# Kernel tuning notes

Measured on AMD Instinct MI355X. Metric: run time of the kernel, lower is better.

## Reference

```python
import jax, jax.numpy as jnp
import numpy as np

B, S, D, NQ, NC, MC, K = 64, 200, 128, 50000, 1000, 4, 10
N = NQ + NC  # total graph nodes (concepts first, then questions, matching torch concat order)


def setup_inputs() -> dict:
    key = jax.random.key(0)
    ks = jax.random.split(key, 32)
    f = lambda i, shape: jax.random.normal(ks[i], shape, dtype=jnp.float32) * 0.02
    return {
        "emb_q": f(0, (NQ, D)), "emb_c": f(1, (NC, D)), "emb_r": f(2, (2, D)),
        "Wih1": f(3, (3 * D, 2 * D)), "Whh1": f(4, (3 * D, D)), "bih1": f(5, (3 * D,)), "bhh1": f(6, (3 * D,)),
        "Wih2": f(7, (3 * D, D)), "Whh2": f(8, (3 * D, D)), "bih2": f(9, (3 * D,)), "bhh2": f(10, (3 * D,)),
        "Wg1": f(11, (D, D)), "Wg2": f(12, (D, D)), "Wg3": f(13, (D, D)),
        "Wagg": f(14, (D, D)), "bagg": f(15, (D,)),
        "Wq": f(16, (D, D)), "bq": f(17, (D,)),
        "Wk": f(18, (D, D)), "bk": f(19, (D,)),
        "Ww": f(20, (1, 2 * D)), "bw": f(21, (1,)),
        "question_seq": jax.random.randint(ks[22], (B, S), 0, NQ),
        "correct_seq": jax.random.randint(ks[23], (B, S), 0, 2),
        "mask_seq": jnp.ones((B, S), dtype=jnp.int32),
        "q_table": jax.random.randint(ks[24], (NQ, MC), 0, NC),
    }


def _gru(x, h, Wih, Whh, bih, bhh):
    gi = x @ Wih.T + bih
    gh = h @ Whh.T + bhh
    i_r, i_z, i_n = jnp.split(gi, 3, axis=-1)
    h_r, h_z, h_n = jnp.split(gh, 3, axis=-1)
    r = jax.nn.sigmoid(i_r + h_r)
    z = jax.nn.sigmoid(i_z + h_z)
    n = jnp.tanh(i_n + r * h_n)
    return (1.0 - z) * n + z * h


def _sage_mean(x, src, dst, W):
    # SAGEConv4GIKT (eval): out = lin_r(mean_agg_over_neighbors + x), lin_r has no bias.
    agg = jax.ops.segment_sum(x[dst], src, num_segments=N)
    cnt = jax.ops.segment_sum(jnp.ones((src.shape[0], 1), x.dtype), src, num_segments=N)
    agg = agg / jnp.maximum(cnt, 1.0)
    return (agg + x) @ W.T


def reference(emb_q, emb_c, emb_r, Wih1, Whh1, bih1, bhh1, Wih2, Whh2, bih2, bhh2,
              Wg1, Wg2, Wg3, Wagg, bagg, Wq, bq, Wk, bk, Ww, bw,
              question_seq, correct_seq, mask_seq, q_table):
    # ---- GNN propagation over the full question-concept bipartite graph ----
    x = jnp.concatenate([emb_c, emb_q], axis=0)  # [N, D], concepts first
    q_glob = jnp.repeat(jnp.arange(NQ, dtype=q_table.dtype) + NC, MC)  # question global ids
    c_glob = q_table.reshape(-1)                                       # concept global ids
    x = _sage_mean(x, q_glob, c_glob, Wg1)  # q2c: aggregate at questions from concepts
    x = _sage_mean(x, c_glob, q_glob, Wg2)  # c2q: aggregate at concepts from questions
    x = _sage_mean(x, q_glob, c_glob, Wg3)  # q2c again
    x = jnp.tanh(x @ Wagg.T + bagg)

    tgrid = jnp.arange(S)

    def step(carry, inp):
        h1, h2, keyhist, statehist = carry
        t, q_t, r_t, m_t, q_next = inp
        m = (m_t != 0)[:, None]
        e_q = jnp.where(m, x[q_t + NC], emb_q[q_t])  # GNN emb where masked-in, raw emb otherwise
        e_r = emb_r[r_t]
        h1 = _gru(jnp.concatenate([e_q, e_r], axis=1), h1, Wih1, Whh1, bih1, bhh1)
        h2 = _gru(h1, h2, Wih2, Whh2, bih2, bhh2)
        statehist = statehist.at[:, t].set(h2)
        keyhist = keyhist.at[:, t].set(h2 @ Wk.T + bk)
        # queries: next question emb + its concept embs -> [B, MC+1, D]
        qc = jnp.concatenate([emb_q[q_next][:, None, :], emb_c[q_table[q_next]]], axis=1)
        aq = qc @ Wq.T + bq
        scores = jnp.einsum('bid,bjd->bij', aq, keyhist)  # [B, MC+1, S]
        scores = jnp.where((tgrid <= t)[None, None, :], scores, -1e9)
        flat = scores.reshape(B, -1)
        vals, idx = jax.lax.top_k(flat, K)  # top-k (query, state) pairs
        alpha = jax.nn.softmax(vals, axis=-1)
        i_idx = idx // S
        j_idx = idx % S
        q_sel = jnp.take_along_axis(qc, i_idx[:, :, None], axis=1)        # [B, K, D]
        s_sel = jnp.take_along_axis(statehist, j_idx[:, :, None], axis=1)  # [B, K, D]
        f = jax.nn.sigmoid(jnp.concatenate([q_sel, s_sel], axis=-1) @ Ww.T + bw)[..., 0]
        y = jnp.sum(alpha * f, axis=-1)  # [B]
        return (h1, h2, keyhist, statehist), y

    h0 = jnp.zeros((B, D), jnp.float32)
    carry = (h0, h0, jnp.zeros((B, S, D), jnp.float32), jnp.zeros((B, S, D), jnp.float32))
    xs = (jnp.arange(S - 1), question_seq[:, :-1].T, correct_seq[:, :-1].T,
          mask_seq[:, :-1].T, question_seq[:, 1:].T)
    _, ys = jax.lax.scan(step, carry, xs)
    y_hat = jnp.concatenate([jnp.zeros((B, 1), jnp.float32), ys.T], axis=1)  # predictions for t=1..S-1
    return y_hat
```

## Files before the change

### kernel.cpp

```cpp
#include <hip/hip_runtime.h>
#include <math.h>

#define Bz 64
#define Sz 200
#define Dz 128
#define NQz 50000
#define NCz 1000
#define MCz 4
#define Kz 10
#define Tz 199
#define NSz (Bz*Tz)
#define NEz (NQz*MCz)
#define KTpad 256

__global__ void k_count(const int* __restrict__ qt, int* __restrict__ cnt) {
    int e = blockIdx.x*256 + threadIdx.x;
    if (e < NEz) atomicAdd(&cnt[qt[e]], 1);
}

__global__ void k_offs(const int* __restrict__ cnt, int* __restrict__ offs) {
    __shared__ int s[1024];
    int tid = threadIdx.x;
    s[tid] = (tid < NCz) ? cnt[tid] : 0;
    __syncthreads();
    for (int off = 1; off < 1024; off <<= 1) {
        int add = (tid >= off) ? s[tid - off] : 0;
        __syncthreads();
        s[tid] += add;
        __syncthreads();
    }
    if (tid < NCz) offs[tid + 1] = s[tid];
    if (tid == 0) offs[0] = 0;
}

__global__ void k_fill(const int* __restrict__ qt, const int* __restrict__ offs,
                       int* __restrict__ fill, int* __restrict__ edge_q) {
    int e = blockIdx.x*256 + threadIdx.x;
    if (e < NEz) {
        int c = qt[e];
        int pos = atomicAdd(&fill[c], 1);
        edge_q[offs[c] + pos] = e >> 2;
    }
}

__global__ void k_m2(const int* __restrict__ qt, const int* __restrict__ offs,
                     const int* __restrict__ edge_q,
                     const float* __restrict__ emb_q, const float* __restrict__ emb_c,
                     float* __restrict__ m2) {
    int c = blockIdx.x;
    int g = threadIdx.x >> 7;
    int d = threadIdx.x & 127;
    int e0 = offs[c], e1 = offs[c+1];
    float acc = 0.f;
    for (int e = e0 + g; e < e1; e += 4) {
        int q = edge_q[e];
        const int* t4 = qt + q*4;
        int c0 = t4[0], c1 = t4[1], c2 = t4[2], c3 = t4[3];
        acc += emb_q[q*128 + d]
             + 0.25f*(emb_c[c0*128+d] + emb_c[c1*128+d] + emb_c[c2*128+d] + emb_c[c3*128+d]);
    }
    __shared__ float ps[4][128];
    ps[g][d] = acc;
    __syncthreads();
    if (g == 0) {
        float tot = ps[0][d] + ps[1][d] + ps[2][d] + ps[3][d];
        float cn = (float)(e1 - e0);
        m2[c*128 + d] = tot / fmaxf(cn, 1.0f);
    }
}

template<bool TR>
__global__ void k_mm128(const float* __restrict__ X, const float* __restrict__ Y,
                        float* __restrict__ out) {
    int r = blockIdx.x, c = threadIdx.x;
    float acc = 0.f;
    for (int e = 0; e < 128; ++e) acc += X[r*128 + e] * Y[e*128 + c];
    if (TR) out[c*128 + r] = acc;
    else    out[r*128 + c] = acc;
}

__global__ void k_gr(const float* __restrict__ emb_r, const float* __restrict__ Wih1,
                     const float* __restrict__ bih1, float* __restrict__ gr) {
    int rt = threadIdx.x / 384, r = threadIdx.x % 384;
    float acc = bih1[r];
    for (int e = 0; e < 128; ++e) acc += emb_r[rt*128 + e] * Wih1[r*256 + 128 + e];
    gr[rt*384 + r] = acc;
}

__global__ void k_bkq(const float* __restrict__ Wq, const float* __restrict__ Wk,
                      const float* __restrict__ bq, const float* __restrict__ bk,
                      const float* __restrict__ Ww, const float* __restrict__ bw,
                      float* __restrict__ Bkq, float* __restrict__ biaskq) {
    int r = blockIdx.x, d = threadIdx.x;
    if (r < 128) {
        float acc = 0.f;
        for (int n = 0; n < 128; ++n) acc += Wq[n*128 + r] * Wk[n*128 + d];
        Bkq[r*128 + d] = acc;
        if (d == 0) {
            float b0 = 0.f;
            for (int n = 0; n < 128; ++n) b0 += Wq[n*128 + r] * bk[n];
            biaskq[r] = b0;
        }
    } else if (r == 128) {
        float acc = 0.f;
        for (int n = 0; n < 128; ++n) acc += bq[n] * Wk[n*128 + d];
        Bkq[128*128 + d] = acc;
        if (d == 0) {
            float c0 = 0.f;
            for (int n = 0; n < 128; ++n) c0 += bq[n] * bk[n];
            biaskq[128] = c0;
        }
    } else {
        Bkq[129*128 + d] = Ww[128 + d];
        if (d == 0) biaskq[129] = bw[0];
    }
}

__global__ void k_eq(const float* __restrict__ Mt_g, const float* __restrict__ bagg,
                     const float* __restrict__ emb_q, const float* __restrict__ emb_c,
                     const float* __restrict__ m2, const int* __restrict__ qseq,
                     const int* __restrict__ mseq, const int* __restrict__ qt,
                     float* __restrict__ eq) {
    __shared__ float Mt[128*128];
    __shared__ float ub[2][128];
    int tid = threadIdx.x;
    for (int i = tid; i < 128*128/4; i += 256)
        ((float4*)Mt)[i] = ((const float4*)Mt_g)[i];
    __syncthreads();
    int g = tid >> 7, d = tid & 127;
    for (int it = 0; it < 8; ++it) {
        int slot = blockIdx.x*16 + it*2 + g;
        int b = slot / Tz, t = slot % Tz;
        int q = qseq[b*Sz + t];
        int msk = mseq[b*Sz + t];
        if (msk) {
            const int* t4 = qt + q*4;
            int c0 = t4[0], c1 = t4[1], c2 = t4[2], c3 = t4[3];
            ub[g][d] = emb_q[q*128 + d]
                     + 0.5f *(emb_c[c0*128+d] + emb_c[c1*128+d] + emb_c[c2*128+d] + emb_c[c3*128+d])
                     + 0.25f*(m2[c0*128+d]  + m2[c1*128+d]  + m2[c2*128+d]  + m2[c3*128+d]);
        }
        __syncthreads();
        if (msk) {
            float acc = bagg[d];
            const float* urow = ub[g];
            for (int e = 0; e < 128; ++e) acc += Mt[e*128 + d] * urow[e];
            eq[slot*128 + d] = tanhf(acc);
        } else {
            eq[slot*128 + d] = emb_q[q*128 + d];
        }
        __syncthreads();
    }
}

__device__ __forceinline__ float bf_lo(unsigned u){ return __uint_as_float(u << 16); }
__device__ __forceinline__ float bf_hi(unsigned u){ return __uint_as_float(u & 0xffff0000u); }
__device__ __forceinline__ unsigned f2bf(float x){
    unsigned u = __float_as_uint(x);
    return (u + 0x7fffu + ((u >> 16) & 1u)) >> 16;
}
__device__ __forceinline__ unsigned pk2(float a, float b){
    return f2bf(a) | (f2bf(b) << 16);
}
__device__ __forceinline__ float rcpf(float x){ return __builtin_amdgcn_rcpf(x); }
__device__ __forceinline__ float sigm(float x){ return rcpf(1.f + __expf(-x)); }
__device__ __forceinline__ float tanh_fast(float x){
    float e = __expf(2.f*x);
    return 1.f - 2.f*rcpf(e + 1.f);
}

#if __has_builtin(__builtin_amdgcn_fdot2_f32_bf16)
typedef __attribute__((ext_vector_type(2))) short short2v;
__device__ __forceinline__ float bdot2(unsigned w, unsigned h, float acc) {
    return __builtin_amdgcn_fdot2_f32_bf16(__builtin_bit_cast(short2v, w),
                                           __builtin_bit_cast(short2v, h), acc, false);
}
#else
__device__ __forceinline__ float bdot2(unsigned w, unsigned h, float acc) {
    return acc + bf_lo(w)*bf_lo(h) + bf_hi(w)*bf_hi(h);
}
#endif

template<int MODE, int DOT2>
__global__ void k_gemm(const float* __restrict__ A, const float* __restrict__ Bm,
                       int ldb, int nB, float* __restrict__ C, int ldc,
                       const float* __restrict__ bias, const float* __restrict__ gr,
                       const int* __restrict__ cseq) {
    __shared__ int rtb[64];
    int tx = threadIdx.x, ty = threadIdx.y;
    int tid = ty*16 + tx;
    int m0 = blockIdx.x * 64;
    int n0 = blockIdx.y * 64;
    if (MODE == 1 && tid < 64) {
        int s = m0 + tid;
        int b = s / Tz, t = s % Tz;
        rtb[tid] = cseq[b*Sz + t];
    }
    float acc[4][4];
    #pragma unroll
    for (int i = 0; i < 4; ++i)
        #pragma unroll
        for (int j = 0; j < 4; ++j) acc[i][j] = 0.f;

    if (DOT2) {
        __shared__ unsigned As[64][17];
        __shared__ unsigned Bs[64][17];
        for (int kc = 0; kc < 128; kc += 32) {
            #pragma unroll
            for (int l = 0; l < 2; ++l) {
                int v = tid*2 + l;
                int row = v >> 3, c4 = (v & 7) << 2;
                int p0 = (kc + c4) >> 1 & 15;
                float4 av = *(const float4*)(A + (size_t)(m0+row)*128 + kc + c4);
                As[row][p0]   = pk2(av.x, av.y);
                As[row][p0+1] = pk2(av.z, av.w);
                int nrow = n0 + row;
                float4 bv = make_float4(0.f, 0.f, 0.f, 0.f);
                if (nrow < nB) bv = *(const float4*)(Bm + (size_t)nrow*ldb + kc + c4);
                Bs[row][p0]   = pk2(bv.x, bv.y);
                Bs[row][p0+1] = pk2(bv.z, bv.w);
            }
            __syncthreads();
            #pragma unroll 4
            for (int kp = 0; kp < 16; ++kp) {
                unsigned av[4], bv[4];
                #pragma unroll
                for (int i = 0; i < 4; ++i) av[i] = As[ty*4+i][kp];
                #pragma unroll
                for (int j = 0; j < 4; ++j) bv[j] = Bs[tx*4+j][kp];
                #pragma unroll
                for (int i = 0; i < 4; ++i)
                    #pragma unroll
                    for (int j = 0; j < 4; ++j) acc[i][j] = bdot2(av[i], bv[j], acc[i][j]);
            }
            __syncthreads();
        }
    } else {
        __shared__ float Asf[64][33];
        __shared__ float Bsf[64][33];
        for (int kc = 0; kc < 128; kc += 32) {
            #pragma unroll
            for (int l = 0; l < 2; ++l) {
                int v = tid*2 + l;
                int row = v >> 3, c4 = (v & 7) << 2;
                float4 av = *(const float4*)(A + (size_t)(m0+row)*128 + kc + c4);
                Asf[row][c4+0] = av.x; Asf[row][c4+1] = av.y; Asf[row][c4+2] = av.z; Asf[row][c4+3] = av.w;
                int nrow = n0 + row;
                float4 bv = make_float4(0.f, 0.f, 0.f, 0.f);
                if (nrow < nB) bv = *(const float4*)(Bm + (size_t)nrow*ldb + kc + c4);
                Bsf[row][c4+0] = bv.x; Bsf[row][c4+1] = bv.y; Bsf[row][c4+2] = bv.z; Bsf[row][c4+3] = bv.w;
            }
            __syncthreads();
            #pragma unroll 8
            for (int k = 0; k < 32; ++k) {
                float av[4], bv[4];
                #pragma unroll
                for (int i = 0; i < 4; ++i) av[i] = Asf[ty*4+i][k];
                #pragma unroll
                for (int j = 0; j < 4; ++j) bv[j] = Bsf[tx*4+j][k];
                #pragma unroll
                for (int i = 0; i < 4; ++i)
                    #pragma unroll
                    for (int j = 0; j < 4; ++j) acc[i][j] += av[i]*bv[j];
            }
            __syncthreads();
        }
    }
    #pragma unroll
    for (int i = 0; i < 4; ++i) {
        int s = m0 + ty*4 + i;
        if (MODE == 2) {
            int bb = s / Tz, tt = s - ((int)(s / Tz))*Tz;
            #pragma unroll
            for (int j = 0; j < 4; ++j) {
                int col = n0 + tx*4 + j;
                if (col < nB)
                    C[((size_t)bb*132 + col)*KTpad + tt] = acc[i][j] + bias[col];
            }
        } else {
            #pragma unroll
            for (int j = 0; j < 4; ++j) {
                int col = n0 + tx*4 + j;
                if (col < nB) {
                    float v = acc[i][j];
                    if (MODE == 0) v += bias[col];
                    else           v += gr[rtb[ty*4+i]*384 + col];
                    C[(size_t)s*ldc + col] = v;
                }
            }
        }
    }
}

__global__ void __launch_bounds__(384, 1)
k_scan(const float* __restrict__ gi, const float* __restrict__ Whh,
       const float* __restrict__ bhh, float* __restrict__ hout) {
    int b = blockIdx.x, tid = threadIdx.x;

    unsigned w[64];
    {
        const float4* w4 = (const float4*)(Whh + (size_t)tid*128);
        #pragma unroll
        for (int k = 0; k < 32; ++k) {
            float4 v = w4[k];
            w[2*k] = pk2(v.x, v.y); w[2*k+1] = pk2(v.z, v.w);
        }
    }
    float bb = bhh[tid];

    __shared__ unsigned hb[64];
    __shared__ float gh[384];
    if (tid < 64) hb[tid] = 0u;

    float g0=0.f,g1=0.f,g2=0.f,g3=0.f,g4=0.f,g5=0.f;
    if (tid < 64) {
        const float2* gp = (const float2*)(gi + (size_t)(b*Tz)*384);
        float2 x0 = gp[tid], x1 = gp[tid+64], x2 = gp[tid+128];
        g0=x0.x; g1=x0.y; g2=x1.x; g3=x1.y; g4=x2.x; g5=x2.y;
    }
    __syncthreads();

    const uint4* hv = (const uint4*)hb;

    for (int t = 0; t < Tz; ++t) {
        float n0=0.f,n1=0.f,n2=0.f,n3=0.f,n4=0.f,n5=0.f;
        if (tid < 64 && t + 1 < Tz) {
            const float2* gp = (const float2*)(gi + (size_t)(b*Tz + t + 1)*384);
            float2 x0 = gp[tid], x1 = gp[tid+64], x2 = gp[tid+128];
            n0=x0.x; n1=x0.y; n2=x1.x; n3=x1.y; n4=x2.x; n5=x2.y;
        }
        float a0=0.f, a1=0.f, a2=0.f, a3=0.f;
        #pragma unroll
        for (int k = 0; k < 8; ++k) {
            uint4 hp = hv[k];
            a0 = bdot2(w[4*k+0], hp.x, a0);
            a1 = bdot2(w[4*k+1], hp.y, a1);
            a2 = bdot2(w[4*k+2], hp.z, a2);
            a3 = bdot2(w[4*k+3], hp.w, a3);
        }
        gh[tid] = bb + ((a0+a1)+(a2+a3));
        __syncthreads();
        if (tid < 64) {
            int u = 2*tid;
            unsigned hp = hb[tid];
            float r0 = sigm(g0 + gh[u]);
            float r1 = sigm(g1 + gh[u+1]);
            float z0 = sigm(g2 + gh[u+128]);
            float z1 = sigm(g3 + gh[u+129]);
            float q0 = tanh_fast(g4 + r0*gh[u+256]);
            float q1 = tanh_fast(g5 + r1*gh[u+257]);
            float h0  = (1.f - z0)*q0 + z0*bf_lo(hp);
            float h1v = (1.f - z1)*q1 + z1*bf_hi(hp);
            hb[tid] = pk2(h0, h1v);
            ((float2*)(hout + (size_t)(b*Tz + t)*128))[tid] = make_float2(h0, h1v);
        }
        g0=n0; g1=n1; g2=n2; g3=n3; g4=n4; g5=n5;
        __syncthreads();
    }
}

__global__ void __launch_bounds__(256, 1)
k_attn(const float* __restrict__ kqt, const int* __restrict__ qseq,
       const int* __restrict__ qt, const float* __restrict__ emb_q,
       const float* __restrict__ emb_c, const float* __restrict__ Ww,
       float* __restrict__ out) {
    int wid  = threadIdx.x >> 6;
    int lane = threadIdx.x & 63;
    int b = blockIdx.y;
    int t = blockIdx.x*4 + wid;
    if (t > Tz - 1) t = Tz - 1;

    __shared__ float qc[4][5][128];
    __shared__ float gqs[4][5];
    int qn = qseq[b*Sz + t + 1];
    for (int idx = lane; idx < 5*128; idx += 64) {
        int i = idx / 128, d = idx & 127;
        const float* src = (i == 0) ? (emb_q + (size_t)qn*128)
                                    : (emb_c + (size_t)qt[qn*4 + (i-1)]*128);
        qc[wid][i][d] = src[d];
    }
    __syncthreads();
    {
        float w0 = Ww[lane], w1 = Ww[lane + 64];
        #pragma unroll
        for (int i = 0; i < 5; ++i) {
            float p = qc[wid][i][lane]*w0 + qc[wid][i][lane+64]*w1;
            #pragma unroll
            for (int off = 32; off >= 1; off >>= 1) p += __shfl_xor(p, off);
            if (lane == 0) gqs[wid][i] = p;
        }
    }
    __syncthreads();

    const float* base = kqt + (size_t)b*(132*KTpad);

    float acc[4][5];
    #pragma unroll
    for (int jj = 0; jj < 4; ++jj)
        #pragma unroll
        for (int i = 0; i < 5; ++i) acc[jj][i] = 0.f;

    #pragma unroll 2
    for (int c = 0; c < 32; ++c) {
        float4 k0 = ((const float4*)(base + (size_t)(4*c+0)*KTpad))[lane];
        float4 k1 = ((const float4*)(base + (size_t)(4*c+1)*KTpad))[lane];
        float4 k2 = ((const float4*)(base + (size_t)(4*c+2)*KTpad))[lane];
        float4 k3 = ((const float4*)(base + (size_t)(4*c+3)*KTpad))[lane];
        #pragma unroll
        for (int i = 0; i < 5; ++i) {
            float4 q = ((const float4*)qc[wid][i])[c];
            acc[0][i] += q.x*k0.x + q.y*k1.x + q.z*k2.x + q.w*k3.x;
            acc[1][i] += q.x*k0.y + q.y*k1.y + q.z*k2.y + q.w*k3.y;
            acc[2][i] += q.x*k0.z + q.y*k1.z + q.z*k2.z + q.w*k3.z;
            acc[3][i] += q.x*k0.w + q.y*k1.w + q.z*k2.w + q.w*k3.w;
        }
    }

    const float NEG = -3.402823466e38f;
    float sv[10]; int si[10];
    #pragma unroll
    for (int k = 0; k < 10; ++k) { sv[k] = NEG; si[k] = 0x7FFFFFFF; }

    auto ins = [&](float cv, int ci) {
        if (cv > sv[9] || (cv == sv[9] && ci < si[9])) {
            #pragma unroll
            for (int k = 0; k < 10; ++k) {
                bool bet = (cv > sv[k]) || (cv == sv[k] && ci < si[k]);
                float tv = sv[k]; int ti = si[k];
                if (bet) { sv[k] = cv; si[k] = ci; cv = tv; ci = ti; }
            }
        }
    };
    {
        float4 kb4 = ((const float4*)(base + 128*KTpad))[lane];
        float kbv[4] = {kb4.x, kb4.y, kb4.z, kb4.w};
        #pragma unroll
        for (int jj = 0; jj < 4; ++jj) {
            int j = 4*lane + jj;
            if (j <= t) {
                #pragma unroll
                for (int i = 0; i < 5; ++i) ins(acc[jj][i] + kbv[jj], i*Sz + j);
            }
        }
    }

    float vmax = 0.f, myv = 0.f; int myidx = 0x7FFFFFFF;
    #pragma unroll
    for (int rnd = 0; rnd < 10; ++rnd) {
        float v = sv[0]; int idx = si[0];
        #pragma unroll
        for (int off = 32; off >= 1; off >>= 1) {
            float ov = __shfl_xor(v, off);
            int   oi = __shfl_xor(idx, off);
            if (ov > v || (ov == v && oi < idx)) { v = ov; idx = oi; }
        }
        if (rnd == 0) vmax = v;
        if (lane == rnd) { myv = v; myidx = idx; }
        if (si[0] == idx) {
            #pragma unroll
            for (int k = 0; k < 9; ++k) { sv[k] = sv[k+1]; si[k] = si[k+1]; }
            sv[9] = NEG; si[9] = 0x7FFFFFFF;
        }
    }

    float num = 0.f, den = 0.f;
    if (lane < 10 && myidx != 0x7FFFFFFF) {
        float a = __expf(myv - vmax);
        int ik = myidx / Sz, jk = myidx % Sz;
        float gsj = base[129*KTpad + jk];
        float f = sigm(gqs[wid][ik] + gsj);
        num = a*f; den = a;
    }
    #pragma unroll
    for (int off = 32; off >= 1; off >>= 1) {
        num += __shfl_xor(num, off);
        den += __shfl_xor(den, off);
    }
    if (lane == 0) out[b*Sz + t + 1] = num/den;
}

static inline size_t alup(size_t x) { return (x + 255) & ~(size_t)255; }

extern "C" void kernel_launch(void* const* d_in, const int* in_sizes, int n_in,
                              void* d_out, int out_size, void* d_ws, size_t ws_size,
                              hipStream_t stream) {
    (void)in_sizes; (void)n_in; (void)ws_size;
    const float* emb_q = (const float*)d_in[0];
    const float* emb_c = (const float*)d_in[1];
    const float* emb_r = (const float*)d_in[2];
    const float* Wih1  = (const float*)d_in[3];
    const float* Whh1  = (const float*)d_in[4];
    const float* bih1  = (const float*)d_in[5];
    const float* bhh1  = (const float*)d_in[6];
    const float* Wih2  = (const float*)d_in[7];
    const float* Whh2  = (const float*)d_in[8];
    const float* bih2  = (const float*)d_in[9];
    const float* bhh2  = (const float*)d_in[10];
    const float* Wg1   = (const float*)d_in[11];
    const float* Wg2   = (const float*)d_in[12];
    const float* Wg3   = (const float*)d_in[13];
    const float* Wagg  = (const float*)d_in[14];
    const float* bagg  = (const float*)d_in[15];
    const float* Wq    = (const float*)d_in[16];
    const float* bq    = (const float*)d_in[17];
    const float* Wk    = (const float*)d_in[18];
    const float* bk    = (const float*)d_in[19];
    const float* Ww    = (const float*)d_in[20];
    const float* bw    = (const float*)d_in[21];
    const int* qseq    = (const int*)d_in[22];
    const int* cseq    = (const int*)d_in[23];
    const int* mseq    = (const int*)d_in[24];
    const int* qtab    = (const int*)d_in[25];
    float* out = (float*)d_out;

    char* p = (char*)d_ws;
    auto alloc = [&](size_t bytes) { char* r = p; p += alup(bytes); return r; };
    int*   cnt    = (int*)  alloc(4096);
    int*   fill   = (int*)  alloc(4096);
    int*   offs   = (int*)  alloc(1001*4);
    int*   edge_q = (int*)  alloc((size_t)NEz*4);
    float* m2     = (float*)alloc((size_t)NCz*128*4);
    float* T1     = (float*)alloc(128*128*4);
    float* T2     = (float*)alloc(128*128*4);
    float* Mt     = (float*)alloc(128*128*4);
    float* gr     = (float*)alloc(2*384*4);
    float* Bkq    = (float*)alloc(132*128*4);
    float* biaskq = (float*)alloc(132*4);
    float* eq     = (float*)alloc((size_t)NSz*128*4);
    float* gi1    = (float*)alloc((size_t)NSz*384*4);
    float* stateh = (float*)alloc((size_t)NSz*128*4);
    float* kqt    = (float*)alloc((size_t)Bz*132*KTpad*4);
    float* h1all = eq;
    float* gi2   = gi1;

    hipMemsetAsync(cnt, 0, 8192, stream);
    hipMemsetAsync(d_out, 0, (size_t)out_size*4, stream);

    k_count<<<(NEz+255)/256, 256, 0, stream>>>(qtab, cnt);
    k_offs <<<1, 1024, 0, stream>>>(cnt, offs);
    k_fill <<<(NEz+255)/256, 256, 0, stream>>>(qtab, offs, fill, edge_q);
    k_m2   <<<NCz, 512, 0, stream>>>(qtab, offs, edge_q, emb_q, emb_c, m2);

    k_mm128<false><<<128, 128, 0, stream>>>(Wg2, Wg1, T1);
    k_mm128<false><<<128, 128, 0, stream>>>(Wg3, T1, T2);
    k_mm128<true> <<<128, 128, 0, stream>>>(Wagg, T2, Mt);
    k_gr  <<<1, 768, 0, stream>>>(emb_r, Wih1, bih1, gr);
    k_bkq <<<130, 128, 0, stream>>>(Wq, Wk, bq, bk, Ww, bw, Bkq, biaskq);

    k_eq  <<<NSz/16, 256, 0, stream>>>(Mt, bagg, emb_q, emb_c, m2, qseq, mseq, qtab, eq);

    k_gemm<1,1><<<dim3(NSz/64, 6), dim3(16,16), 0, stream>>>(eq, Wih1, 256, 384,
                                                             gi1, 384, nullptr, gr, cseq);
    k_scan<<<Bz, 384, 0, stream>>>(gi1, Whh1, bhh1, h1all);
    k_gemm<0,1><<<dim3(NSz/64, 6), dim3(16,16), 0, stream>>>(h1all, Wih2, 128, 384,
                                                             gi2, 384, bih2, nullptr, nullptr);
    k_scan<<<Bz, 384, 0, stream>>>(gi2, Whh2, bhh2, stateh);

    k_gemm<2,0><<<dim3(NSz/64, 3), dim3(16,16), 0, stream>>>(stateh, Bkq, 128, 132,
                                                             kqt, 0, biaskq, nullptr, nullptr);
    k_attn<<<dim3((Tz+3)/4, Bz), 256, 0, stream>>>(kqt, qseq, qtab, emb_q, emb_c, Ww, out);
}
```

Baseline: 683.7 us.

## Process two batch rows per GRU scan block and use packed FMA in attention

The GRU recurrence kernel now handles two batch sequences per block. Each thread reuses its register-resident bf16 weights for two hidden-state dot products, and the launch is halved to 32 blocks. This amortizes the per-step barrier and latency over twice the work, at the cost of using only half as many CUs, which lengthens each step's critical path. Separately, the attention score accumulation is rewritten with inline v_pk_fma_f32 assembly to issue two FMAs per instruction.

After: 718.9 us. 5.1% more time.

```diff
diff --git a/kernel.cpp b/kernel.cpp
--- a/kernel.cpp
+++ b/kernel.cpp
@@ -181,6 +181,16 @@
 }
 #endif
 
+typedef __attribute__((ext_vector_type(2))) float v2f;
+__device__ __forceinline__ void pkfma_lo(v2f &acc, v2f k, v2f q) {
+    asm("v_pk_fma_f32 %0, %1, %2, %0 op_sel_hi:[1,0,1]"
+        : "+v"(acc) : "v"(k), "v"(q));
+}
+__device__ __forceinline__ void pkfma_hi(v2f &acc, v2f k, v2f q) {
+    asm("v_pk_fma_f32 %0, %1, %2, %0 op_sel:[0,1,0] op_sel_hi:[1,1,1]"
+        : "+v"(acc) : "v"(k), "v"(q));
+}
+
 template<int MODE, int DOT2>
 __global__ void k_gemm(const float* __restrict__ A, const float* __restrict__ Bm,
                        int ldb, int nB, float* __restrict__ C, int ldc,
@@ -295,7 +305,7 @@
 __global__ void __launch_bounds__(384, 1)
 k_scan(const float* __restrict__ gi, const float* __restrict__ Whh,
        const float* __restrict__ bhh, float* __restrict__ hout) {
-    int b = blockIdx.x, tid = threadIdx.x;
+    int b0 = blockIdx.x*2, tid = threadIdx.x;
 
     unsigned w[64];
     {
@@ -308,51 +318,63 @@
     }
     float bb = bhh[tid];
 
-    __shared__ unsigned hb[64];
-    __shared__ float gh[384];
-    if (tid < 64) hb[tid] = 0u;
+    __shared__ unsigned hb[2][64];
+    __shared__ float gh[2][384];
+    if (tid < 128) hb[tid>>6][tid&63] = 0u;
 
     float g0=0.f,g1=0.f,g2=0.f,g3=0.f,g4=0.f,g5=0.f;
-    if (tid < 64) {
-        const float2* gp = (const float2*)(gi + (size_t)(b*Tz)*384);
-        float2 x0 = gp[tid], x1 = gp[tid+64], x2 = gp[tid+128];
+    if (tid < 128) {
+        const float2* gp = (const float2*)(gi + (size_t)((b0 + (tid>>6))*Tz)*384);
+        int u = tid & 63;
+        float2 x0 = gp[u], x1 = gp[u+64], x2 = gp[u+128];
         g0=x0.x; g1=x0.y; g2=x1.x; g3=x1.y; g4=x2.x; g5=x2.y;
     }
     __syncthreads();
 
-    const uint4* hv = (const uint4*)hb;
+    const uint4* hv0 = (const uint4*)hb[0];
+    const uint4* hv1 = (const uint4*)hb[1];
 
     for (int t = 0; t < Tz; ++t) {
         float n0=0.f,n1=0.f,n2=0.f,n3=0.f,n4=0.f,n5=0.f;
-        if (tid < 64 && t + 1 < Tz) {
-            const float2* gp = (const float2*)(gi + (size_t)(b*Tz + t + 1)*384);
-            float2 x0 = gp[tid], x1 = gp[tid+64], x2 = gp[tid+128];
+        if (tid < 128 && t + 1 < Tz) {
+            const float2* gp = (const float2*)(gi + (size_t)((b0 + (tid>>6))*Tz + t + 1)*384);
+            int u = tid & 63;
+            float2 x0 = gp[u], x1 = gp[u+64], x2 = gp[u+128];
             n0=x0.x; n1=x0.y; n2=x1.x; n3=x1.y; n4=x2.x; n5=x2.y;
         }
         float a0=0.f, a1=0.f, a2=0.f, a3=0.f;
+        float c0=0.f, c1=0.f, c2=0.f, c3=0.f;
         #pragma unroll
         for (int k = 0; k < 8; ++k) {
-            uint4 hp = hv[k];
+            uint4 hp = hv0[k];
+            uint4 hq = hv1[k];
             a0 = bdot2(w[4*k+0], hp.x, a0);
             a1 = bdot2(w[4*k+1], hp.y, a1);
             a2 = bdot2(w[4*k+2], hp.z, a2);
             a3 = bdot2(w[4*k+3], hp.w, a3);
-        }
-        gh[tid] = bb + ((a0+a1)+(a2+a3));
+            c0 = bdot2(w[4*k+0], hq.x, c0);
+            c1 = bdot2(w[4*k+1], hq.y, c1);
+            c2 = bdot2(w[4*k+2], hq.z, c2);
+            c3 = bdot2(w[4*k+3], hq.w, c3);
+        }
+        gh[0][tid] = bb + ((a0+a1)+(a2+a3));
+        gh[1][tid] = bb + ((c0+c1)+(c2+c3));
         __syncthreads();
-        if (tid < 64) {
-            int u = 2*tid;
-            unsigned hp = hb[tid];
-            float r0 = sigm(g0 + gh[u]);
-            float r1 = sigm(g1 + gh[u+1]);
-            float z0 = sigm(g2 + gh[u+128]);
-            float z1 = sigm(g3 + gh[u+129]);
-            float q0 = tanh_fast(g4 + r0*gh[u+256]);
-            float q1 = tanh_fast(g5 + r1*gh[u+257]);
+        if (tid < 128) {
+            int ch = tid >> 6;
+            int u = 2*(tid & 63);
+            unsigned hp = hb[ch][tid & 63];
+            const float* ghc = gh[ch];
+            float r0 = sigm(g0 + ghc[u]);
+            float r1 = sigm(g1 + ghc[u+1]);
+            float z0 = sigm(g2 + ghc[u+128]);
+            float z1 = sigm(g3 + ghc[u+129]);
+            float q0 = tanh_fast(g4 + r0*ghc[u+256]);
+            float q1 = tanh_fast(g5 + r1*ghc[u+257]);
             float h0  = (1.f - z0)*q0 + z0*bf_lo(hp);
             float h1v = (1.f - z1)*q1 + z1*bf_hi(hp);
-            hb[tid] = pk2(h0, h1v);
-            ((float2*)(hout + (size_t)(b*Tz + t)*128))[tid] = make_float2(h0, h1v);
+            hb[ch][tid & 63] = pk2(h0, h1v);
+            ((float2*)(hout + (size_t)((b0+ch)*Tz + t)*128))[tid & 63] = make_float2(h0, h1v);
         }
         g0=n0; g1=n1; g2=n2; g3=n3; g4=n4; g5=n5;
         __syncthreads();
@@ -394,11 +416,9 @@
 
     const float* base = kqt + (size_t)b*(132*KTpad);
 
-    float acc[4][5];
+    v2f accA[5], accB[5];
     #pragma unroll
-    for (int jj = 0; jj < 4; ++jj)
-        #pragma unroll
-        for (int i = 0; i < 5; ++i) acc[jj][i] = 0.f;
+    for (int i = 0; i < 5; ++i) { accA[i] = (v2f){0.f,0.f}; accB[i] = (v2f){0.f,0.f}; }
 
     #pragma unroll 2
     for (int c = 0; c < 32; ++c) {
@@ -406,13 +426,18 @@
         float4 k1 = ((const float4*)(base + (size_t)(4*c+1)*KTpad))[lane];
         float4 k2 = ((const float4*)(base + (size_t)(4*c+2)*KTpad))[lane];
         float4 k3 = ((const float4*)(base + (size_t)(4*c+3)*KTpad))[lane];
+        v2f k0a = {k0.x,k0.y}, k0b = {k0.z,k0.w};
+        v2f k1a = {k1.x,k1.y}, k1b = {k1.z,k1.w};
+        v2f k2a = {k2.x,k2.y}, k2b = {k2.z,k2.w};
+        v2f k3a = {k3.x,k3.y}, k3b = {k3.z,k3.w};
         #pragma unroll
         for (int i = 0; i < 5; ++i) {
             float4 q = ((const float4*)qc[wid][i])[c];
-            acc[0][i] += q.x*k0.x + q.y*k1.x + q.z*k2.x + q.w*k3.x;
-            acc[1][i] += q.x*k0.y + q.y*k1.y + q.z*k2.y + q.w*k3.y;
-            acc[2][i] += q.x*k0.z + q.y*k1.z + q.z*k2.z + q.w*k3.z;
-            acc[3][i] += q.x*k0.w + q.y*k1.w + q.z*k2.w + q.w*k3.w;
+            v2f qa = {q.x,q.y}, qb = {q.z,q.w};
+            pkfma_lo(accA[i], k0a, qa); pkfma_lo(accB[i], k0b, qa);
+            pkfma_hi(accA[i], k1a, qa); pkfma_hi(accB[i], k1b, qa);
+            pkfma_lo(accA[i], k2a, qb); pkfma_lo(accB[i], k2b, qb);
+            pkfma_hi(accA[i], k3a, qb); pkfma_hi(accB[i], k3b, qb);
         }
     }
 
@@ -439,7 +464,11 @@
             int j = 4*lane + jj;
             if (j <= t) {
                 #pragma unroll
-                for (int i = 0; i < 5; ++i) ins(acc[jj][i] + kbv[jj], i*Sz + j);
+                for (int i = 0; i < 5; ++i) {
+                    float a = (jj == 0) ? accA[i].x : (jj == 1) ? accA[i].y
+                            : (jj == 2) ? accB[i].x : accB[i].y;
+                    ins(a + kbv[jj], i*Sz + j);
+                }
             }
         }
     }
@@ -551,10 +580,10 @@
 
     k_gemm<1,1><<<dim3(NSz/64, 6), dim3(16,16), 0, stream>>>(eq, Wih1, 256, 384,
                                                              gi1, 384, nullptr, gr, cseq);
-    k_scan<<<Bz, 384, 0, stream>>>(gi1, Whh1, bhh1, h1all);
+    k_scan<<<Bz/2, 384, 0, stream>>>(gi1, Whh1, bhh1, h1all);
     k_gemm<0,1><<<dim3(NSz/64, 6), dim3(16,16), 0, stream>>>(h1all, Wih2, 128, 384,
                                                              gi2, 384, bih2, nullptr, nullptr);
-    k_scan<<<Bz, 384, 0, stream>>>(gi2, Whh2, bhh2, stateh);
+    k_scan<<<Bz/2, 384, 0, stream>>>(gi2, Whh2, bhh2, stateh);
 
     k_gemm<2,0><<<dim3(NSz/64, 3), dim3(16,16), 0, stream>>>(stateh, Bkq, 128, 132,
                                                              kqt, 0, biaskq, nullptr, nullptr);
```
